# Kernel tuning notes

Hardware: AMD Instinct MI355X
Metric: run time of the kernel (lower is better)

Reference implementation:

```python
import jax, jax.numpy as jnp
import numpy as np

SCENE = (128, 128, 8)      # (X, Y, Z) voxel grid
VOXEL_SIZE = 0.4
DOWNSAMPLE_Z = 2
NUM_HEADS = 8
NUM_POINTS = 4
LN_EPS = 1e-5


def _pix2vox(depth, K, E, voxel_origin):
    # depth [1,H,W]; K [1,3,3]; E [1,4,4]; voxel_origin [1,3]
    B, H, W = depth.shape
    gx, gy = jnp.meshgrid(jnp.arange(W, dtype=depth.dtype), jnp.arange(H, dtype=depth.dtype))
    pix = jnp.stack([gx, gy])                              # [2,H,W] -> (u, v) after flip in torch
    d = depth[:, None]                                     # [B,1,H,W]
    p_x = jnp.concatenate([pix[None] * d, d], 1).reshape(B, 3, -1)
    p_c = jnp.linalg.inv(K) @ p_x                          # camera coords [B,3,HW]
    p_c = jnp.concatenate([p_c, jnp.ones_like(p_c[:, :1])], 1)
    p_w = jnp.linalg.inv(E) @ p_c                          # world coords [B,4,HW]
    p_v = (jnp.swapaxes(p_w[:, :3], 1, 2) - voxel_origin[:, None, :]) / VOXEL_SIZE - 0.5
    p_v = p_v.at[..., 2].set(p_v[..., 2] / DOWNSAMPLE_Z)
    return jnp.trunc(p_v).astype(jnp.int32)               # torch .long() truncates toward 0


def _voxel_mask(p_v):
    X, Y, Z = SCENE
    p = p_v[0]                                             # [HW,3] (batch asserted == 1)
    valid = ((p[:, 0] >= 0) & (p[:, 0] < X) & (p[:, 1] >= 0) & (p[:, 1] < Y)
             & (p[:, 2] >= 0) & (p[:, 2] < Z))
    flat = jnp.where(valid, (p[:, 0] * Y + p[:, 1]) * Z + p[:, 2], 0)
    return jnp.zeros(X * Y * Z, dtype=bool).at[flat].max(valid)


def _ms_deform_attn(q, feats, ref, Wv, bv, Woff, boff, Wattw, battw, Wout, bout):
    # q [N,C]; feats: list of [C,Hl,Wl]; ref [N,2] normalized (shared across levels)
    N, C = q.shape
    hd = C // NUM_HEADS
    shapes = [(f.shape[1], f.shape[2]) for f in feats]
    L = len(feats)
    flat = jnp.concatenate([f.reshape(C, -1).T for f in feats], 0)      # [Lsum, C]
    value = (flat @ Wv.T + bv).reshape(-1, NUM_HEADS, hd)               # [Lsum, h, hd]
    off = (q @ Woff.T + boff).reshape(N, NUM_HEADS, L, NUM_POINTS, 2)
    w = jax.nn.softmax((q @ Wattw.T + battw).reshape(N, NUM_HEADS, L * NUM_POINTS), -1)
    w = w.reshape(N, NUM_HEADS, L, NUM_POINTS)
    normalizer = jnp.array([[wl, hl] for (hl, wl) in shapes], dtype=q.dtype)  # (W,H) per level
    loc = ref[:, None, None, None, :] + off / normalizer[None, None, :, None, :]
    h_idx = jnp.arange(NUM_HEADS)[None, :, None]
    out = jnp.zeros((N, NUM_HEADS, hd), q.dtype)
    start = 0
    for lvl, (Hl, Wl) in enumerate(shapes):
        v = value[start:start + Hl * Wl]                   # [Hl*Wl, h, hd]
        start += Hl * Wl
        # grid_sample bilinear, align_corners=False, zero padding
        x = loc[:, :, lvl, :, 0] * Wl - 0.5                # [N,h,P]
        y = loc[:, :, lvl, :, 1] * Hl - 0.5
        x0 = jnp.floor(x); y0 = jnp.floor(y)
        lx = x - x0; ly = y - y0
        x0i = x0.astype(jnp.int32); y0i = y0.astype(jnp.int32)
        samp = jnp.zeros((N, NUM_HEADS, NUM_POINTS, hd), q.dtype)
        for dy, dx, wgt in ((0, 0, (1 - lx) * (1 - ly)), (0, 1, lx * (1 - ly)),
                            (1, 0, (1 - lx) * ly), (1, 1, lx * ly)):
            xi = x0i + dx; yi = y0i + dy
            ok = (xi >= 0) & (xi < Wl) & (yi >= 0) & (yi < Hl)
            idx = jnp.where(ok, yi * Wl + xi, 0)
            g = v[idx, h_idx]                              # [N,h,P,hd] per-head gather
            samp = samp + g * (wgt * ok)[..., None]
        out = out + jnp.einsum('nhp,nhpd->nhd', w[:, :, lvl], samp)
    return out.reshape(N, C) @ Wout.T + bout


def _forward(scene_embed, feat0, feat1, feat2, depth, K, E, voxel_origin, ref_pix,
             Wv, bv, Woff, boff, Wattw, battw, Wout, bout, ln_g, ln_b):
    X, Y, Z = SCENE
    mask = _voxel_mask(_pix2vox(depth, K, E, voxel_origin))             # [N] bool
    q = scene_embed[0]                                                  # [N,C]
    attn = _ms_deform_attn(q, [feat0[0], feat1[0], feat2[0]], ref_pix[0],
                           Wv, bv, Woff, boff, Wattw, battw, Wout, bout)
    h = q + attn                                                        # residual (MSDeformAttn identity)
    mu = jnp.mean(h, -1, keepdims=True)
    var = jnp.mean((h - mu) ** 2, -1, keepdims=True)
    h = (h - mu) / jnp.sqrt(var + LN_EPS) * ln_g + ln_b                 # post-norm
    out = jnp.where(mask[:, None], h, q)                                # index_fov_back_to_voxels
    return out.T.reshape(1, -1, X, Y, Z)                                # nlc -> nchw [1,C,X,Y,Z]


def setup_inputs() -> dict:
    key = jax.random.key(0)
    ks = jax.random.split(key, 12)
    X, Y, Z = SCENE
    N = X * Y * Z
    C = 128
    H, W = 192, 640
    s = 0.02
    scene_embed = jax.random.normal(ks[0], (1, N, C), jnp.float32)
    feat0 = jax.random.normal(ks[1], (1, C, 48, 160), jnp.float32)
    feat1 = jax.random.normal(ks[2], (1, C, 24, 80), jnp.float32)
    feat2 = jax.random.normal(ks[3], (1, C, 12, 40), jnp.float32)
    depth = jax.random.uniform(ks[4], (1, H, W), jnp.float32, 1.0, 40.0)
    K = jnp.array([[[552.55, 0.0, 320.0], [0.0, 552.55, 96.0], [0.0, 0.0, 1.0]]], jnp.float32)
    E = jnp.eye(4, dtype=jnp.float32)[None]
    voxel_origin = jnp.array([[-25.6, -3.2, 0.0]], jnp.float32)
    ref_pix = jax.random.uniform(ks[5], (1, N, 2), jnp.float32)
    return {
        'scene_embed': scene_embed, 'feat0': feat0, 'feat1': feat1, 'feat2': feat2,
        'depth': depth, 'K': K, 'E': E, 'voxel_origin': voxel_origin, 'ref_pix': ref_pix,
        'Wv': jax.random.normal(ks[6], (C, C), jnp.float32) * s,
        'bv': jnp.zeros((C,), jnp.float32),
        'Woff': jax.random.normal(ks[7], (NUM_HEADS * 3 * NUM_POINTS * 2, C), jnp.float32) * s,
        'boff': jnp.zeros((NUM_HEADS * 3 * NUM_POINTS * 2,), jnp.float32),
        'Wattw': jax.random.normal(ks[8], (NUM_HEADS * 3 * NUM_POINTS, C), jnp.float32) * s,
        'battw': jnp.zeros((NUM_HEADS * 3 * NUM_POINTS,), jnp.float32),
        'Wout': jax.random.normal(ks[9], (C, C), jnp.float32) * s,
        'bout': jnp.zeros((C,), jnp.float32),
        'ln_g': jnp.ones((C,), jnp.float32),
        'ln_b': jnp.zeros((C,), jnp.float32),
    }


def reference(scene_embed, feat0, feat1, feat2, depth, K, E, voxel_origin, ref_pix,
              Wv, bv, Woff, boff, Wattw, battw, Wout, bout, ln_g, ln_b):
    return _forward(scene_embed, feat0, feat1, feat2, depth, K, E, voxel_origin, ref_pix,
                    Wv, bv, Woff, boff, Wattw, battw, Wout, bout, ln_g, ln_b)
```

## Files before the change

kernel.cpp:

```cpp
#include <hip/hip_runtime.h>
#include <hip/hip_bf16.h>
#include <stdint.h>

#define XS 128
#define YS 128
#define ZS 8
#define NQ (XS*YS*ZS)
#define CDIM 128
#define NH 8
#define HD 16
#define DH 192
#define DW 640
#define NPIX (DH*DW)
#define NVPIX 10080

typedef float f32x4 __attribute__((ext_vector_type(4)));
typedef short s16x8 __attribute__((ext_vector_type(8)));

__device__ __forceinline__ float b2f(unsigned short u){
    union { unsigned int i; float f; } v; v.i = ((unsigned int)u) << 16; return v.f;
}
__device__ __forceinline__ unsigned short f2b(float f){
    __hip_bfloat16 h = __float2bfloat16(f);
    return *reinterpret_cast<unsigned short*>(&h);
}
__device__ __forceinline__ float blo(unsigned int u){
    union { unsigned int i; float f; } v; v.i = u << 16; return v.f;
}
__device__ __forceinline__ float bhi(unsigned int u){
    union { unsigned int i; float f; } v; v.i = u & 0xffff0000u; return v.f;
}

__global__ __launch_bounds__(256)
void inv_kernel(const float* __restrict__ K,
                const float* __restrict__ E,
                double* __restrict__ inv_out,
                const float* __restrict__ Woff,
                const float* __restrict__ Wattw,
                const float* __restrict__ Wout,
                unsigned short* __restrict__ Wbf){
    if (blockIdx.x != 0){
        int idx = (blockIdx.x-1)*256 + threadIdx.x;
        if (idx < 24576)      Wbf[idx] = f2b(Woff[idx]);
        else if (idx < 36864) Wbf[idx] = f2b(Wattw[idx-24576]);
        else if (idx < 40960) Wbf[idx] = 0;
        else if (idx < 57344) Wbf[idx] = f2b(Wout[idx-40960]);
        return;
    }
    if (threadIdx.x != 0) return;
    double k[3][3], e[4][4];
    for (int i=0;i<9;i++)  k[i/3][i%3] = (double)K[i];
    for (int i=0;i<16;i++) e[i/4][i%4] = (double)E[i];
    double det = k[0][0]*(k[1][1]*k[2][2]-k[1][2]*k[2][1])
               - k[0][1]*(k[1][0]*k[2][2]-k[1][2]*k[2][0])
               + k[0][2]*(k[1][0]*k[2][1]-k[1][1]*k[2][0]);
    double id = 1.0/det;
    double inv[3][3];
    inv[0][0]=(k[1][1]*k[2][2]-k[1][2]*k[2][1])*id;
    inv[0][1]=(k[0][2]*k[2][1]-k[0][1]*k[2][2])*id;
    inv[0][2]=(k[0][1]*k[1][2]-k[0][2]*k[1][1])*id;
    inv[1][0]=(k[1][2]*k[2][0]-k[1][0]*k[2][2])*id;
    inv[1][1]=(k[0][0]*k[2][2]-k[0][2]*k[2][0])*id;
    inv[1][2]=(k[0][2]*k[1][0]-k[0][0]*k[1][2])*id;
    inv[2][0]=(k[1][0]*k[2][1]-k[1][1]*k[2][0])*id;
    inv[2][1]=(k[0][1]*k[2][0]-k[0][0]*k[2][1])*id;
    inv[2][2]=(k[0][0]*k[1][1]-k[0][1]*k[1][0])*id;
    for (int i=0;i<9;i++) inv_out[i] = inv[i/3][i%3];
    double a[4][8];
    for (int i=0;i<4;i++){ for(int j=0;j<4;j++){ a[i][j]=e[i][j]; a[i][4+j]=(i==j)?1.0:0.0; } }
    for (int c=0;c<4;c++){
        int piv=c; double best=fabs(a[c][c]);
        for (int r=c+1;r<4;r++){ double v=fabs(a[r][c]); if (v>best){best=v;piv=r;} }
        if (piv!=c){ for (int j=0;j<8;j++){ double tmp=a[c][j]; a[c][j]=a[piv][j]; a[piv][j]=tmp; } }
        double pv = 1.0/a[c][c];
        for (int j=0;j<8;j++) a[c][j]*=pv;
        for (int r=0;r<4;r++){
            if (r==c) continue;
            double f=a[r][c];
            for(int j=0;j<8;j++) a[r][j]-=f*a[c][j];
        }
    }
    for (int i=0;i<16;i++) inv_out[9+i] = a[i/4][4 + (i%4)];
}

__global__ __launch_bounds__(256)
void prep2_kernel(int nVal,
                  const float* __restrict__ f0,
                  const float* __restrict__ f1,
                  const float* __restrict__ f2,
                  const float* __restrict__ Wv,
                  const float* __restrict__ bv,
                  unsigned short* __restrict__ value,
                  const float* __restrict__ depth,
                  const double* __restrict__ invm,
                  const float* __restrict__ vorigin,
                  unsigned char* __restrict__ mask){
    __shared__ float fl2[2][CDIM][4];
    const int t = threadIdx.x;
    if ((int)blockIdx.x < nVal){
        const int half = t >> 7, tt = t & 127;
        const int p0 = blockIdx.x*8 + half*4;
        float (*fl)[4] = fl2[half];
        const float* src; int hw, lp;
        if (p0 < 7680)      { src=f0; hw=7680; lp=p0; }
        else if (p0 < 9600) { src=f1; hw=1920; lp=p0-7680; }
        else                { src=f2; hw=480;  lp=p0-9600; }
        float4 v = *(const float4*)(src + tt*hw + lp);
        fl[tt][0]=v.x; fl[tt][1]=v.y; fl[tt][2]=v.z; fl[tt][3]=v.w;
        __syncthreads();
        float bb = bv[tt];
        float acc[4] = {bb,bb,bb,bb};
        const float4* wrow = (const float4*)(Wv + tt*CDIM);
        #pragma unroll 8
        for (int kc=0; kc<32; ++kc){
            float4 w = wrow[kc];
            #pragma unroll
            for (int u=0;u<4;u++){
                float wu = (u==0)?w.x:(u==1)?w.y:(u==2)?w.z:w.w;
                float4 fv = *(const float4*)fl[kc*4+u];
                acc[0] += fv.x*wu; acc[1] += fv.y*wu; acc[2] += fv.z*wu; acc[3] += fv.w*wu;
            }
        }
        const int hh = tt >> 4, cc = tt & 15;
        #pragma unroll
        for (int i=0;i<4;i++)
            value[((size_t)hh*NVPIX + (size_t)(p0+i))*HD + cc] = f2b(acc[i]);
    } else {
        int tid = (blockIdx.x - nVal)*256 + t;
        if (tid >= NPIX) return;
        int gx = tid % DW, gy = tid / DW;
        double d  = (double)depth[tid];
        double X0 = (double)gx * d, X1 = (double)gy * d, X2 = d;
        double c0 = invm[0]*X0 + invm[1]*X1 + invm[2]*X2;
        double c1 = invm[3]*X0 + invm[4]*X1 + invm[5]*X2;
        double c2 = invm[6]*X0 + invm[7]*X1 + invm[8]*X2;
        const double* iE = invm + 9;
        double w0 = iE[0]*c0 + iE[1]*c1 + iE[2]*c2  + iE[3];
        double w1 = iE[4]*c0 + iE[5]*c1 + iE[6]*c2  + iE[7];
        double w2 = iE[8]*c0 + iE[9]*c1 + iE[10]*c2 + iE[11];
        double v0 = (w0-(double)vorigin[0])/0.4 - 0.5;
        double v1 = (w1-(double)vorigin[1])/0.4 - 0.5;
        double v2 = ((w2-(double)vorigin[2])/0.4 - 0.5) / 2.0;
        int xi = (int)v0, yi = (int)v1, zi = (int)v2;
        if (xi>=0 && xi<XS && yi>=0 && yi<YS && zi>=0 && zi<ZS)
            mask[(xi*YS + yi)*ZS + zi] = 1;
    }
}

__global__ __launch_bounds__(256, 2)
void attn_fused(const float* __restrict__ q_in,
                const float* __restrict__ refpix,
                const unsigned short* __restrict__ Wbf,
                const float* __restrict__ boff,
                const float* __restrict__ battw,
                const unsigned short* __restrict__ value,
                const unsigned short* __restrict__ WoutBf,
                const float* __restrict__ bout,
                const float* __restrict__ lng,
                const float* __restrict__ lnb,
                const unsigned char* __restrict__ mask,
                float* __restrict__ dout){
    const int n0g = blockIdx.x * 8;
    const int t = threadIdx.x;
    __shared__ __align__(16) unsigned char smem[25296];
    unsigned short* Ob    = (unsigned short*)(smem);
    unsigned char*  qbfB  = smem + 4608;
    float*          bias  = (float*)(smem + 6656);
    unsigned char*  descB = smem + 4608;
    float*          out2  = (float*)(smem + 4608);
    unsigned char*  obfB  = smem + 16896;
    float (*q_s)[CDIM]    = (float(*)[CDIM])(smem + 20992);
    float*          rp_s  = (float*)(smem + 25088);
    float*          wredp = (float*)(smem + 25152);
    unsigned char*  mask_s= (unsigned char*)(smem + 25280);

    {
        float4 qv = ((const float4*)(q_in + (size_t)n0g*CDIM))[t];
        ((float4*)q_s)[t] = qv;
        const int q = t >> 5;
        unsigned int pk0 = (unsigned int)f2b(qv.x) | ((unsigned int)f2b(qv.y)<<16);
        unsigned int pk1 = (unsigned int)f2b(qv.z) | ((unsigned int)f2b(qv.w)<<16);
        unsigned int bo = (unsigned int)(q*256 + (t&31)*8) ^ (unsigned int)(q<<4);
        *(unsigned int*)(qbfB + bo)     = pk0;
        *(unsigned int*)(qbfB + bo + 4) = pk1;
        for (int i=t;i<288;i+=256) bias[i] = (i<192)? boff[i] : battw[i-192];
        ((unsigned int*)obfB)[512 + t] = 0;
        ((unsigned int*)obfB)[768 + t] = 0;
        if (t < 16) rp_s[t] = refpix[n0g*2 + t];
        if (t < 8)  mask_s[t] = mask[n0g + t];
    }
    __syncthreads();

    {
        const int w = t >> 6, lane = t & 63, lr = lane & 15, lg = lane >> 4;
        const int q = lr & 7;
        const int nt0 = w*5;
        f32x4 acc[5];
        #pragma unroll
        for (int i=0;i<5;i++) acc[i] = (f32x4){0.f,0.f,0.f,0.f};
        #pragma unroll
        for (int ks=0; ks<4; ++ks){
            s16x8 bfrag = *(const s16x8*)(qbfB + (((unsigned int)(q*256 + ks*64 + lg*16)) ^ (unsigned int)(q<<4)));
            const unsigned short* wp = Wbf + (size_t)(nt0*16 + lr)*CDIM + ks*32 + lg*8;
            #pragma unroll
            for (int j=0;j<5;++j){
                s16x8 af = *(const s16x8*)(wp + j*16*CDIM);
                acc[j] = __builtin_amdgcn_mfma_f32_16x16x32_bf16(af, bfrag, acc[j], 0, 0, 0);
            }
        }
        if (lr < 8){
            #pragma unroll
            for (int j=0;j<5;++j){
                int nt = nt0 + j;
                if (nt < 18){
                    #pragma unroll
                    for (int r=0;r<4;++r){
                        int f = nt*16 + lg*4 + r;
                        Ob[f*8 + lr] = f2b(acc[j][r] + bias[f]);
                    }
                }
            }
        }
    }
    __syncthreads();

    if (t < 64){
        int q = t >> 3, h = t & 7;
        unsigned short* p = Ob + (192 + h*12)*8 + q;
        float e[12]; float m = -1e30f;
        #pragma unroll
        for (int i=0;i<12;i++){ e[i] = b2f(p[i*8]); m = fmaxf(m, e[i]); }
        float s = 0.f;
        #pragma unroll
        for (int i=0;i<12;i++){ e[i] = __expf(e[i]-m); s += e[i]; }
        float is = 1.f/s;
        #pragma unroll
        for (int i=0;i<12;i++) p[i*8] = f2b(e[i]*is);
    }
    __syncthreads();

    for (int idx = t; idx < 768; idx += 256){
        int q = idx & 7, hp = idx >> 3;
        int lp = hp % 12;
        float fw, fh; int Wl, Hl, st;
        if (lp < 4)      { fw=160.f; fh=48.f; Wl=160; Hl=48; st=0; }
        else if (lp < 8) { fw=80.f;  fh=24.f; Wl=80;  Hl=24; st=7680; }
        else             { fw=40.f;  fh=12.f; Wl=40;  Hl=12; st=9600; }
        float offx = b2f(Ob[(hp*2)*8 + q]);
        float offy = b2f(Ob[(hp*2+1)*8 + q]);
        float aw   = b2f(Ob[(192+hp)*8 + q]);
        float x = rp_s[q*2+0]*fw - 0.5f + offx;
        float y = rp_s[q*2+1]*fh - 0.5f + offy;
        float x0f = floorf(x), y0f = floorf(y);
        float lx = x-x0f, ly = y-y0f;
        int x0 = (int)x0f, y0 = (int)y0f;
        bool x0ok = (x0>=0)&&(x0<Wl), x1ok=(x0+1>=0)&&(x0+1<Wl);
        bool y0ok = (y0>=0)&&(y0<Hl), y1ok=(y0+1>=0)&&(y0+1<Hl);
        float w00 = (x0ok&&y0ok)? (1.f-lx)*(1.f-ly)*aw : 0.f;
        float w01 = (x1ok&&y0ok)? lx*(1.f-ly)*aw       : 0.f;
        float w10 = (x0ok&&y1ok)? (1.f-lx)*ly*aw       : 0.f;
        float w11 = (x1ok&&y1ok)? lx*ly*aw             : 0.f;
        int yc0 = min(max(y0,0),Hl-1), yc1 = min(max(y0+1,0),Hl-1);
        int xc0 = min(max(x0,0),Wl-1), xc1 = min(max(x0+1,0),Wl-1);
        unsigned int rb0 = (unsigned int)(st + yc0*Wl), rb1 = (unsigned int)(st + yc1*Wl);
        uint4 d;
        d.x = (rb0+(unsigned int)xc0) | ((rb0+(unsigned int)xc1)<<16);
        d.y = (rb1+(unsigned int)xc0) | ((rb1+(unsigned int)xc1)<<16);
        d.z = (unsigned int)f2b(w00) | ((unsigned int)f2b(w01)<<16);
        d.w = (unsigned int)f2b(w10) | ((unsigned int)f2b(w11)<<16);
        *(uint4*)(descB + (((unsigned int)(idx ^ ((idx>>5)&7)))<<4)) = d;
    }
    __syncthreads();

    {
        const int cp = t & 7, hs = (t>>3) & 7, qgs = t >> 6;
        const unsigned short* vh = value + ((size_t)hs*NVPIX)*HD + cp*2;
        float av0x=0.f, av0y=0.f, av1x=0.f, av1y=0.f;
        #pragma unroll
        for (int lp=0; lp<12; ++lp){
            #pragma unroll
            for (int qi2=0; qi2<2; ++qi2){
                int idx = (hs*12+lp)*8 + qgs*2 + qi2;
                uint4 d = *(const uint4*)(descB + (((unsigned int)(idx ^ ((idx>>5)&7)))<<4));
                unsigned int p00 = d.x & 0xffffu, p01 = d.x >> 16;
                unsigned int p10 = d.y & 0xffffu, p11 = d.y >> 16;
                unsigned int u00 = *(const unsigned int*)(vh + (p00<<4));
                unsigned int u01 = *(const unsigned int*)(vh + (p01<<4));
                unsigned int u10 = *(const unsigned int*)(vh + (p10<<4));
                unsigned int u11 = *(const unsigned int*)(vh + (p11<<4));
                float w00 = blo(d.z), w01 = bhi(d.z), w10 = blo(d.w), w11 = bhi(d.w);
                float sx = blo(u00)*w00 + blo(u01)*w01 + blo(u10)*w10 + blo(u11)*w11;
                float sy = bhi(u00)*w00 + bhi(u01)*w01 + bhi(u10)*w10 + bhi(u11)*w11;
                if (qi2 == 0){ av0x += sx; av0y += sy; }
                else         { av1x += sx; av1y += sy; }
            }
        }
        const int q0q = qgs*2;
        unsigned int pk0 = (unsigned int)f2b(av0x) | ((unsigned int)f2b(av0y)<<16);
        unsigned int pk1 = (unsigned int)f2b(av1x) | ((unsigned int)f2b(av1y)<<16);
        unsigned int bo0 = (unsigned int)(q0q*256 + hs*32 + cp*4)     ^ (unsigned int)((q0q&7)<<4);
        unsigned int bo1 = (unsigned int)((q0q+1)*256 + hs*32 + cp*4) ^ (unsigned int)(((q0q+1)&7)<<4);
        *(unsigned int*)(obfB + bo0) = pk0;
        *(unsigned int*)(obfB + bo1) = pk1;
    }
    __syncthreads();

    {
        const int w = t >> 6, lane = t & 63, lr = lane & 15, lg = lane >> 4;
        f32x4 a0 = (f32x4){0.f,0.f,0.f,0.f};
        f32x4 a1 = (f32x4){0.f,0.f,0.f,0.f};
        #pragma unroll
        for (int ks=0; ks<4; ++ks){
            unsigned int bo = (unsigned int)(lr*256 + ks*64 + lg*16) ^ (unsigned int)((lr&7)<<4);
            s16x8 bfrag = *(const s16x8*)(obfB + bo);
            const unsigned short* wp = WoutBf + (size_t)(w*32 + lr)*CDIM + ks*32 + lg*8;
            s16x8 af0 = *(const s16x8*)(wp);
            s16x8 af1 = *(const s16x8*)(wp + 16*CDIM);
            a0 = __builtin_amdgcn_mfma_f32_16x16x32_bf16(af0, bfrag, a0, 0, 0, 0);
            a1 = __builtin_amdgcn_mfma_f32_16x16x32_bf16(af1, bfrag, a1, 0, 0, 0);
        }
        if (lr < 8){
            int f0 = w*32 + lg*4;
            float4 b0 = *(const float4*)(bout + f0);
            float4 b1 = *(const float4*)(bout + f0 + 16);
            float4 v0, v1;
            v0.x = a0[0]+b0.x; v0.y = a0[1]+b0.y; v0.z = a0[2]+b0.z; v0.w = a0[3]+b0.w;
            v1.x = a1[0]+b1.x; v1.y = a1[1]+b1.y; v1.z = a1[2]+b1.z; v1.w = a1[3]+b1.w;
            *(float4*)(out2 + lr*CDIM + f0)      = v0;
            *(float4*)(out2 + lr*CDIM + f0 + 16) = v1;
        }
    }
    __syncthreads();

    const int r = t & 127;
    const int qb = t >> 7;
    const int wv = t >> 6;
    float acc[4];
    #pragma unroll
    for (int qi4=0;qi4<4;qi4++) acc[qi4] = out2[(qb*4+qi4)*CDIM + r];

    float hv[4], sred[4];
    #pragma unroll
    for (int qi4=0;qi4<4;qi4++){ hv[qi4] = q_s[qb*4+qi4][r] + acc[qi4]; sred[qi4]=hv[qi4]; }
    #pragma unroll
    for (int off=32; off>0; off>>=1)
        #pragma unroll
        for (int qi4=0;qi4<4;qi4++) sred[qi4] += __shfl_xor(sred[qi4], off, 64);
    if ((t&63)==0){
        #pragma unroll
        for (int qi4=0;qi4<4;qi4++) wredp[0*16 + wv*4 + qi4]=sred[qi4];
    }
    __syncthreads();
    float mu[4], dv[4];
    #pragma unroll
    for (int qi4=0;qi4<4;qi4++){
        mu[qi4] = (wredp[0*16 + (qb*2)*4 + qi4]+wredp[0*16 + (qb*2+1)*4 + qi4]) * (1.f/128.f);
        dv[qi4] = hv[qi4]-mu[qi4];
        sred[qi4] = dv[qi4]*dv[qi4];
    }
    #pragma unroll
    for (int off=32; off>0; off>>=1)
        #pragma unroll
        for (int qi4=0;qi4<4;qi4++) sred[qi4] += __shfl_xor(sred[qi4], off, 64);
    if ((t&63)==0){
        #pragma unroll
        for (int qi4=0;qi4<4;qi4++) wredp[1*16 + wv*4 + qi4]=sred[qi4];
    }
    __syncthreads();

    float res[4];
    const float g = lng[r], b = lnb[r];
    #pragma unroll
    for (int qi4=0;qi4<4;qi4++){
        float var = (wredp[1*16 + (qb*2)*4 + qi4]+wredp[1*16 + (qb*2+1)*4 + qi4]) * (1.f/128.f);
        float nv  = dv[qi4] * __frsqrt_rn(var + 1e-5f) * g + b;
        res[qi4] = mask_s[qb*4+qi4] ? nv : q_s[qb*4+qi4][r];
    }
    float4 o; o.x=res[0]; o.y=res[1]; o.z=res[2]; o.w=res[3];
    *(float4*)(dout + (size_t)r*NQ + n0g + qb*4) = o;
}

extern "C" void kernel_launch(void* const* d_in, const int* in_sizes, int n_in,
                              void* d_out, int out_size, void* d_ws, size_t ws_size,
                              hipStream_t stream){
    const float* scene  = (const float*)d_in[0];
    const float* f0     = (const float*)d_in[1];
    const float* f1     = (const float*)d_in[2];
    const float* f2     = (const float*)d_in[3];
    const float* depth  = (const float*)d_in[4];
    const float* K      = (const float*)d_in[5];
    const float* E      = (const float*)d_in[6];
    const float* vorig  = (const float*)d_in[7];
    const float* refpix = (const float*)d_in[8];
    const float* Wv     = (const float*)d_in[9];
    const float* bv     = (const float*)d_in[10];
    const float* Woff   = (const float*)d_in[11];
    const float* boff   = (const float*)d_in[12];
    const float* Wattw  = (const float*)d_in[13];
    const float* battw  = (const float*)d_in[14];
    const float* Wout   = (const float*)d_in[15];
    const float* bout   = (const float*)d_in[16];
    const float* lng    = (const float*)d_in[17];
    const float* lnb    = (const float*)d_in[18];

    char* ws = (char*)d_ws;
    double*         invm   = (double*)(ws);
    unsigned char*  mask   = (unsigned char*)(ws + 512);
    unsigned short* value  = (unsigned short*)(ws + 512 + 131072);
    unsigned short* Wbf    = (unsigned short*)(ws + 512 + 131072 + 2580480);
    unsigned short* WoutBf = Wbf + 40960;

    hipMemsetAsync(mask, 0, NQ, stream);
    inv_kernel<<<225, 256, 0, stream>>>(K, E, invm, Woff, Wattw, Wout, Wbf);

    int nVal  = NVPIX/8;
    int nMask = (NPIX+255)/256;
    prep2_kernel<<<nVal + nMask, 256, 0, stream>>>(nVal, f0, f1, f2, Wv, bv, value,
                                                   depth, invm, vorig, mask);
    attn_fused<<<NQ/8, 256, 0, stream>>>(scene, refpix, Wbf, boff, battw, value,
                                         WoutBf, bout, lng, lnb, mask,
                                         (float*)d_out);
}
```

Measured before the change: 491.5 us.

## Split offset/attention-weight projection into separate 64-query kernel with chunked workspace

Moves the query projection (offsets and attention weights) and its softmax out of the fused attention kernel into a separate kernel. Each block of the new kernel handles 64 queries, so every weight fragment loaded feeds four MFMAs instead of one. Before, lanes 8-15 computed on a query tile only half filled. The results are written as bf16 to a workspace buffer, processed in chunks sized to the available workspace, and read back by the attention kernel. This costs an extra global round trip and possibly several launches.

```diff
diff --git a/kernel.cpp b/kernel.cpp
--- a/kernel.cpp
+++ b/kernel.cpp
@@ -147,25 +147,117 @@
     }
 }
 
-__global__ __launch_bounds__(256, 2)
-void attn_fused(const float* __restrict__ q_in,
-                const float* __restrict__ refpix,
+__global__ __launch_bounds__(256)
+void prep_offaw(const float* __restrict__ q_in,
                 const unsigned short* __restrict__ Wbf,
                 const float* __restrict__ boff,
                 const float* __restrict__ battw,
-                const unsigned short* __restrict__ value,
-                const unsigned short* __restrict__ WoutBf,
-                const float* __restrict__ bout,
-                const float* __restrict__ lng,
-                const float* __restrict__ lnb,
-                const unsigned char* __restrict__ mask,
-                float* __restrict__ dout){
-    const int n0g = blockIdx.x * 8;
+                unsigned short* __restrict__ offawB){
+    __shared__ __align__(16) unsigned char smem[54400];
+    unsigned short* Ob   = (unsigned short*)smem;
+    unsigned char*  qbfB = smem + 36864;
+    float*          bias = (float*)(smem + 53248);
+    const int t = threadIdx.x;
+    const int n0 = blockIdx.x * 64;
+
+    #pragma unroll
+    for (int i=0;i<8;i++){
+        int idx = t + i*256;
+        int row = idx >> 5, c4 = idx & 31;
+        float4 qv = ((const float4*)(q_in + (size_t)(n0+row)*CDIM))[c4];
+        unsigned int pk0 = (unsigned int)f2b(qv.x) | ((unsigned int)f2b(qv.y)<<16);
+        unsigned int pk1 = (unsigned int)f2b(qv.z) | ((unsigned int)f2b(qv.w)<<16);
+        unsigned int bo = ((unsigned int)(row*256 + c4*8)) ^ (unsigned int)((row&7)<<4);
+        *(unsigned int*)(qbfB + bo)     = pk0;
+        *(unsigned int*)(qbfB + bo + 4) = pk1;
+    }
+    for (int i=t;i<288;i+=256) bias[i] = (i<192)? boff[i] : battw[i-192];
+    __syncthreads();
+
+    const int w = t >> 6, lane = t & 63, lr = lane & 15, lg = lane >> 4;
+    const int nt0 = w*5;
+    f32x4 acc[5][4];
+    #pragma unroll
+    for (int j=0;j<5;j++)
+        #pragma unroll
+        for (int qt=0;qt<4;qt++) acc[j][qt] = (f32x4){0.f,0.f,0.f,0.f};
+
+    #pragma unroll
+    for (int ks=0; ks<4; ++ks){
+        s16x8 bf[4];
+        #pragma unroll
+        for (int qt=0;qt<4;qt++){
+            int qrow = qt*16 + lr;
+            unsigned int bo = ((unsigned int)(qrow*256 + ks*64 + lg*16)) ^ (unsigned int)((qrow&7)<<4);
+            bf[qt] = *(const s16x8*)(qbfB + bo);
+        }
+        const unsigned short* wp = Wbf + (size_t)(nt0*16 + lr)*CDIM + ks*32 + lg*8;
+        #pragma unroll
+        for (int j=0;j<5;++j){
+            s16x8 af = *(const s16x8*)(wp + j*16*CDIM);
+            #pragma unroll
+            for (int qt=0;qt<4;qt++)
+                acc[j][qt] = __builtin_amdgcn_mfma_f32_16x16x32_bf16(af, bf[qt], acc[j][qt], 0, 0, 0);
+        }
+    }
+
+    #pragma unroll
+    for (int j=0;j<5;++j){
+        int nt = nt0 + j;
+        if (nt < 18){
+            #pragma unroll
+            for (int qt=0;qt<4;qt++){
+                int q = qt*16 + lr;
+                int base = (q>>3)*2304 + (q&7);
+                #pragma unroll
+                for (int r=0;r<4;++r){
+                    int f = nt*16 + lg*4 + r;
+                    Ob[base + f*8] = f2b(acc[j][qt][r] + bias[f]);
+                }
+            }
+        }
+    }
+    __syncthreads();
+
+    for (int task = t; task < 512; task += 256){
+        int q = task >> 3, h = task & 7;
+        unsigned short* p = Ob + (q>>3)*2304 + (192 + h*12)*8 + (q&7);
+        float e[12]; float m = -1e30f;
+        #pragma unroll
+        for (int i=0;i<12;i++){ e[i] = b2f(p[i*8]); m = fmaxf(m, e[i]); }
+        float s = 0.f;
+        #pragma unroll
+        for (int i=0;i<12;i++){ e[i] = __expf(e[i]-m); s += e[i]; }
+        float is = 1.f/s;
+        #pragma unroll
+        for (int i=0;i<12;i++) p[i*8] = f2b(e[i]*is);
+    }
+    __syncthreads();
+
+    {
+        const uint4* src = (const uint4*)Ob;
+        uint4* dst = (uint4*)(offawB + (size_t)blockIdx.x * 18432);
+        for (int idx = t; idx < 2304; idx += 256) dst[idx] = src[idx];
+    }
+}
+
+__global__ __launch_bounds__(256, 2)
+void attn_kernel(const float* __restrict__ q_in,
+                 const float* __restrict__ refpix,
+                 const unsigned short* __restrict__ offawB,
+                 const unsigned short* __restrict__ value,
+                 const unsigned short* __restrict__ WoutBf,
+                 const float* __restrict__ bout,
+                 const float* __restrict__ lng,
+                 const float* __restrict__ lnb,
+                 const unsigned char* __restrict__ mask,
+                 float* __restrict__ dout,
+                 int q0g){
+    const int n0l = blockIdx.x * 8;
+    const int n0g = q0g + n0l;
     const int t = threadIdx.x;
     __shared__ __align__(16) unsigned char smem[25296];
-    unsigned short* Ob    = (unsigned short*)(smem);
-    unsigned char*  qbfB  = smem + 4608;
-    float*          bias  = (float*)(smem + 6656);
+    unsigned short* raw   = (unsigned short*)(smem);
     unsigned char*  descB = smem + 4608;
     float*          out2  = (float*)(smem + 4608);
     unsigned char*  obfB  = smem + 16896;
@@ -175,67 +267,15 @@
     unsigned char*  mask_s= (unsigned char*)(smem + 25280);
 
     {
-        float4 qv = ((const float4*)(q_in + (size_t)n0g*CDIM))[t];
-        ((float4*)q_s)[t] = qv;
-        const int q = t >> 5;
-        unsigned int pk0 = (unsigned int)f2b(qv.x) | ((unsigned int)f2b(qv.y)<<16);
-        unsigned int pk1 = (unsigned int)f2b(qv.z) | ((unsigned int)f2b(qv.w)<<16);
-        unsigned int bo = (unsigned int)(q*256 + (t&31)*8) ^ (unsigned int)(q<<4);
-        *(unsigned int*)(qbfB + bo)     = pk0;
-        *(unsigned int*)(qbfB + bo + 4) = pk1;
-        for (int i=t;i<288;i+=256) bias[i] = (i<192)? boff[i] : battw[i-192];
+        const unsigned int* src = (const unsigned int*)(offawB + (size_t)(n0l>>3)*2304);
+        unsigned int* dst = (unsigned int*)raw;
+        #pragma unroll
+        for (int i=0;i<5;i++){ int idx = t + i*256; if (idx < 1152) dst[idx] = src[idx]; }
+        ((float4*)q_s)[t] = ((const float4*)(q_in + (size_t)n0g*CDIM))[t];
         ((unsigned int*)obfB)[512 + t] = 0;
         ((unsigned int*)obfB)[768 + t] = 0;
         if (t < 16) rp_s[t] = refpix[n0g*2 + t];
         if (t < 8)  mask_s[t] = mask[n0g + t];
-    }
-    __syncthreads();
-
-    {
-        const int w = t >> 6, lane = t & 63, lr = lane & 15, lg = lane >> 4;
-        const int q = lr & 7;
-        const int nt0 = w*5;
-        f32x4 acc[5];
-        #pragma unroll
-        for (int i=0;i<5;i++) acc[i] = (f32x4){0.f,0.f,0.f,0.f};
-        #pragma unroll
-        for (int ks=0; ks<4; ++ks){
-            s16x8 bfrag = *(const s16x8*)(qbfB + (((unsigned int)(q*256 + ks*64 + lg*16)) ^ (unsigned int)(q<<4)));
-            const unsigned short* wp = Wbf + (size_t)(nt0*16 + lr)*CDIM + ks*32 + lg*8;
-            #pragma unroll
-            for (int j=0;j<5;++j){
-                s16x8 af = *(const s16x8*)(wp + j*16*CDIM);
-                acc[j] = __builtin_amdgcn_mfma_f32_16x16x32_bf16(af, bfrag, acc[j], 0, 0, 0);
-            }
-        }
-        if (lr < 8){
-            #pragma unroll
-            for (int j=0;j<5;++j){
-                int nt = nt0 + j;
-                if (nt < 18){
-                    #pragma unroll
-                    for (int r=0;r<4;++r){
-                        int f = nt*16 + lg*4 + r;
-                        Ob[f*8 + lr] = f2b(acc[j][r] + bias[f]);
-                    }
-                }
-            }
-        }
-    }
-    __syncthreads();
-
-    if (t < 64){
-        int q = t >> 3, h = t & 7;
-        unsigned short* p = Ob + (192 + h*12)*8 + q;
-        float e[12]; float m = -1e30f;
-        #pragma unroll
-        for (int i=0;i<12;i++){ e[i] = b2f(p[i*8]); m = fmaxf(m, e[i]); }
-        float s = 0.f;
-        #pragma unroll
-        for (int i=0;i<12;i++){ e[i] = __expf(e[i]-m); s += e[i]; }
-        float is = 1.f/s;
-        #pragma unroll
-        for (int i=0;i<12;i++) p[i*8] = f2b(e[i]*is);
     }
     __syncthreads();
 
@@ -246,9 +286,9 @@
         if (lp < 4)      { fw=160.f; fh=48.f; Wl=160; Hl=48; st=0; }
         else if (lp < 8) { fw=80.f;  fh=24.f; Wl=80;  Hl=24; st=7680; }
         else             { fw=40.f;  fh=12.f; Wl=40;  Hl=12; st=9600; }
-        float offx = b2f(Ob[(hp*2)*8 + q]);
-        float offy = b2f(Ob[(hp*2+1)*8 + q]);
-        float aw   = b2f(Ob[(192+hp)*8 + q]);
+        float offx = b2f(raw[(hp*2)*8 + q]);
+        float offy = b2f(raw[(hp*2+1)*8 + q]);
+        float aw   = b2f(raw[(192+hp)*8 + q]);
         float x = rp_s[q*2+0]*fw - 0.5f + offx;
         float y = rp_s[q*2+1]*fh - 0.5f + offy;
         float x0f = floorf(x), y0f = floorf(y);
@@ -404,11 +444,19 @@
     const float* lnb    = (const float*)d_in[18];
 
     char* ws = (char*)d_ws;
+    const size_t FIXED = 512 + 131072 + 2580480 + 114688;
     double*         invm   = (double*)(ws);
     unsigned char*  mask   = (unsigned char*)(ws + 512);
     unsigned short* value  = (unsigned short*)(ws + 512 + 131072);
     unsigned short* Wbf    = (unsigned short*)(ws + 512 + 131072 + 2580480);
     unsigned short* WoutBf = Wbf + 40960;
+    unsigned short* offawB = (unsigned short*)(ws + FIXED);
+
+    size_t avail = (ws_size > FIXED) ? (ws_size - FIXED) : 0;
+    long long maxq = (long long)(avail / (288*2));
+    int chunk = (int)((maxq/64)*64);
+    if (chunk > NQ) chunk = NQ;
+    if (chunk < 64) chunk = 64;
 
     hipMemsetAsync(mask, 0, NQ, stream);
     inv_kernel<<<225, 256, 0, stream>>>(K, E, invm, Woff, Wattw, Wout, Wbf);
@@ -417,7 +465,13 @@
     int nMask = (NPIX+255)/256;
     prep2_kernel<<<nVal + nMask, 256, 0, stream>>>(nVal, f0, f1, f2, Wv, bv, value,
                                                    depth, invm, vorig, mask);
-    attn_fused<<<NQ/8, 256, 0, stream>>>(scene, refpix, Wbf, boff, battw, value,
-                                         WoutBf, bout, lng, lnb, mask,
-                                         (float*)d_out);
-}
+
+    for (int q0 = 0; q0 < NQ; q0 += chunk){
+        int len = (NQ - q0 < chunk) ? (NQ - q0) : chunk;
+        prep_offaw<<<len/64, 256, 0, stream>>>(scene + (size_t)q0*CDIM,
+                                               Wbf, boff, battw, offawB);
+        attn_kernel<<<len/8, 256, 0, stream>>>(scene, refpix, offawB, value,
+                                               WoutBf, bout, lng, lnb, mask,
+                                               (float*)d_out, q0);
+    }
+}
```

Result: faster. 418.9 us (-14.8%).
